# Kernel tuning notes

Hardware: AMD Instinct MI355X
Metric: run time of the kernel (lower is better)

The kernel has to match this reference:

```python
import jax, jax.numpy as jnp
import numpy as np

N_NODES = 100000
N_HEDGES = 200000
N_INC = 1000000
N_GRAPHS = 256
H = 64        # h_dim
HE = 35       # hedge_fea_dim
HOUT = 128    # hout_dim
NL = 3        # n_layers
EPS = 1e-5


def _segment_mean(vals, idx, num_segments):
    s = jax.ops.segment_sum(vals, idx, num_segments=num_segments)
    cnt = jax.ops.segment_sum(jnp.ones((vals.shape[0],), vals.dtype), idx,
                              num_segments=num_segments)
    return s / jnp.maximum(cnt, 1.0)[:, None]


def _bn(z, g, b):
    # training-mode BatchNorm1d: batch stats, biased variance
    m = jnp.mean(z, axis=0)
    v = jnp.var(z, axis=0)
    return (z - m) * jax.lax.rsqrt(v + EPS) * g + b


def setup_inputs() -> dict:
    key = jax.random.key(0)
    ks = jax.random.split(key, 32)
    inp = {
        "x": jax.random.normal(ks[0], (N_NODES, 92), jnp.float32),
        "node_idx": jax.random.randint(ks[1], (N_INC,), 0, N_NODES),
        "hedge_idx": jax.random.randint(ks[2], (N_INC,), 0, N_HEDGES),
        "hedge_attr": jax.random.normal(ks[3], (N_HEDGES, HE), jnp.float32),
        "batch": jnp.sort(jax.random.randint(ks[4], (N_NODES,), 0, N_GRAPHS)),
    }
    s = 0.05
    cat = H + HE  # 99
    inp["embed_w"] = jax.random.normal(ks[5], (92, H), jnp.float32) * s
    inp["embed_b"] = jnp.zeros((H,), jnp.float32)
    inp["f1_w"] = jax.random.normal(ks[6], (NL, cat, HE), jnp.float32) * s
    inp["f1_b"] = jnp.zeros((NL, HE), jnp.float32)
    inp["c1_w"] = jax.random.normal(ks[7], (NL, cat, HE), jnp.float32) * s
    inp["c1_b"] = jnp.zeros((NL, HE), jnp.float32)
    inp["f2_w"] = jax.random.normal(ks[8], (NL, cat, H), jnp.float32) * s
    inp["f2_b"] = jnp.zeros((NL, H), jnp.float32)
    inp["c2_w"] = jax.random.normal(ks[9], (NL, cat, H), jnp.float32) * s
    inp["c2_b"] = jnp.zeros((NL, H), jnp.float32)
    inp["bnf_g"] = jnp.ones((NL, HE), jnp.float32)
    inp["bnf_b"] = jnp.zeros((NL, HE), jnp.float32)
    inp["bnc_g"] = jnp.ones((NL, HE), jnp.float32)
    inp["bnc_b"] = jnp.zeros((NL, HE), jnp.float32)
    inp["bno_g"] = jnp.ones((NL, H), jnp.float32)
    inp["bno_b"] = jnp.zeros((NL, H), jnp.float32)
    inp["l2_w"] = jax.random.normal(ks[10], (H, HOUT), jnp.float32) * s
    inp["l2_b"] = jnp.zeros((HOUT,), jnp.float32)
    inp["out_w"] = jax.random.normal(ks[11], (HOUT, 1), jnp.float32) * s
    inp["out_b"] = jnp.zeros((1,), jnp.float32)
    return inp


def reference(x, node_idx, hedge_idx, hedge_attr, batch,
              embed_w, embed_b, f1_w, f1_b, c1_w, c1_b,
              f2_w, f2_b, c2_w, c2_b,
              bnf_g, bnf_b, bnc_g, bnc_b, bno_g, bno_b,
              l2_w, l2_b, out_w, out_b):
    sp = jax.nn.softplus
    x = x @ embed_w + embed_b  # [N, H]
    for i in range(NL):
        # gather node feats per incidence, mean over each hyperedge
        hx = _segment_mean(x[node_idx], hedge_idx, N_HEDGES)       # [NH, H]
        msg = jnp.concatenate([hx, hedge_attr], axis=1)            # [NH, H+HE]
        z_f = _bn(msg @ f1_w[i] + f1_b[i], bnf_g[i], bnf_b[i])
        z_c = _bn(msg @ c1_w[i] + c1_b[i], bnc_g[i], bnc_b[i])
        hedge_attr = jax.nn.sigmoid(z_f) * sp(z_c)                 # [NH, HE]
        z = jnp.concatenate([x[node_idx], hedge_attr[hedge_idx]], axis=-1)  # [E, H+HE]
        o = jax.nn.sigmoid(z @ f2_w[i] + f2_b[i]) * sp(z @ c2_w[i] + c2_b[i])  # [E, H]
        o = _segment_mean(o, node_idx, N_NODES)                    # [N, H]
        o = _bn(o, bno_g[i], bno_b[i])
        x = sp(o + x)
    pooled = _segment_mean(x, batch, N_GRAPHS)                     # [G, H]
    h = sp(pooled @ l2_w + l2_b)                                   # [G, HOUT]
    return h @ out_w + out_b                                       # [G, 1]
```

## Files before the change

### kernel.cpp

```cpp
#include <hip/hip_runtime.h>
#include <math.h>

#define N_NODES 100000
#define N_HEDGES 200000
#define N_INC 1000000
#define N_GRAPHS 256
#define HD 64
#define HE 35
#define CAT 99
#define EPSB 1e-5f

typedef __attribute__((ext_vector_type(8))) short short8;
typedef __attribute__((ext_vector_type(4))) float f32x4;

__device__ __forceinline__ float sp_f(float x) {
  return fmaxf(x, 0.f) + __logf(1.f + __expf(-fabsf(x)));
}
__device__ __forceinline__ float sig_f(float x) {
  return __builtin_amdgcn_rcpf(1.f + __expf(-x));
}
__device__ __forceinline__ unsigned bfr(float x) {
  unsigned u = __float_as_uint(x);
  return (u + 0x7fffu + ((u >> 16) & 1u)) >> 16;
}
__device__ __forceinline__ unsigned pk2(float lo, float hi) {
  return bfr(lo) | (bfr(hi) << 16);
}
__device__ __forceinline__ float blo(unsigned v) { return __uint_as_float(v << 16); }
__device__ __forceinline__ float bhi(unsigned v) {
  return __uint_as_float(v & 0xffff0000u);
}
__device__ __forceinline__ float bf2f(unsigned short s) {
  return __uint_as_float(((unsigned)s) << 16);
}

__global__ __launch_bounds__(256) void k_hist(const int* __restrict__ nidx,
                                              const int* __restrict__ hidx,
                                              int* __restrict__ degN,
                                              int* __restrict__ degH) {
  int e = blockIdx.x * 256 + threadIdx.x;
  if (e >= N_INC) return;
  atomicAdd(&degH[hidx[e]], 1);
  atomicAdd(&degN[nidx[e]], 1);
}

__global__ __launch_bounds__(256) void k_alloc(const int* __restrict__ deg, int n,
                                               int* __restrict__ off,
                                               int* __restrict__ cur,
                                               int* __restrict__ gctr) {
  __shared__ int s[256];
  __shared__ int base;
  int t = threadIdx.x;
  int i = blockIdx.x * 256 + t;
  int d = (i < n) ? deg[i] : 0;
  s[t] = d;
  __syncthreads();
  for (int st = 1; st < 256; st <<= 1) {
    int u = 0;
    if (t >= st) u = s[t - st];
    __syncthreads();
    if (t >= st) s[t] += u;
    __syncthreads();
  }
  if (t == 255) base = atomicAdd(gctr, s[255]);
  __syncthreads();
  int ex = s[t] - d + base;
  if (i < n) {
    off[i] = ex;
    cur[i] = ex;
  }
}

__global__ __launch_bounds__(256) void k_fill(const int* __restrict__ nidx,
                                              const int* __restrict__ hidx,
                                              int* __restrict__ curH,
                                              int* __restrict__ curN,
                                              int* __restrict__ permHn,
                                              int* __restrict__ permNh) {
  int e = blockIdx.x * 256 + threadIdx.x;
  if (e >= N_INC) return;
  int nd = nidx[e], hg = hidx[e];
  int p = atomicAdd(&curH[hg], 1);
  permHn[p] = nd;
  int q = atomicAdd(&curN[nd], 1);
  permNh[q] = hg;
}

__global__ __launch_bounds__(64) void k_wpack(const float* __restrict__ f1w,
                                              const float* __restrict__ c1w,
                                              uint4* __restrict__ wpk) {
  int b = blockIdx.x;
  int layer = b / 20, rem = b % 20, ct = rem / 4, ks = rem % 4;
  int lane = threadIdx.x;
  int col = ct * 16 + (lane & 15);
  int k0 = ks * 32 + (lane >> 4) * 8;
  const float* wf = f1w + layer * CAT * HE;
  const float* wc = c1w + layer * CAT * HE;
  unsigned v[4];
#pragma unroll
  for (int p = 0; p < 4; ++p) {
    float lo = 0.f, hi = 0.f;
    int ka = k0 + p * 2, kb = ka + 1;
    if (ka < 99) {
      if (col < 35) lo = wf[ka * 35 + col];
      else if (col >= 36 && col < 71) lo = wc[ka * 35 + (col - 36)];
    }
    if (kb < 99) {
      if (col < 35) hi = wf[kb * 35 + col];
      else if (col >= 36 && col < 71) hi = wc[kb * 35 + (col - 36)];
    }
    v[p] = pk2(lo, hi);
  }
  uint4 o;
  o.x = v[0]; o.y = v[1]; o.z = v[2]; o.w = v[3];
  wpk[b * 64 + lane] = o;
}

__global__ __launch_bounds__(256) void k_cvt_ha(const float* __restrict__ src,
                                                unsigned short* __restrict__ dst,
                                                int n) {
  int t = blockIdx.x * 256 + threadIdx.x;
  if (t < n) dst[t] = (unsigned short)bfr(src[t]);
}

__global__ __launch_bounds__(256) void k_embed(const float* __restrict__ x,
                                               const float* __restrict__ w,
                                               const float* __restrict__ b,
                                               float* __restrict__ out,
                                               unsigned short* __restrict__ outb) {
  __shared__ float ws[92 * 64];
  __shared__ float rs[16][93];
  int tid = threadIdx.x;
  for (int i = tid; i < 92 * 64; i += 256) ws[i] = w[i];
  int r0 = blockIdx.x * 16;
  for (int i = tid; i < 16 * 92; i += 256) {
    int r = i / 92, k = i - r * 92;
    rs[r][k] = x[(r0 + r) * 92 + k];
  }
  __syncthreads();
  int h = tid & 63;
  float bias = b[h];
  for (int rr = tid >> 6; rr < 16; rr += 4) {
    float acc = bias;
    for (int k = 0; k < 92; ++k) acc += rs[rr][k] * ws[k * 64 + h];
    out[(r0 + rr) * 64 + h] = acc;
    outb[(r0 + rr) * 64 + h] = (unsigned short)bfr(acc);
  }
}

__global__ __launch_bounds__(256) void k_gather_hx(
    const unsigned short* __restrict__ xb, const int* __restrict__ permHn,
    const int* __restrict__ offH, const int* __restrict__ degH,
    unsigned short* __restrict__ hxb) {
  int gt = blockIdx.x * 256 + threadIdx.x;
  int wid = gt >> 6, h = gt & 63;
  if (wid >= N_HEDGES) return;
  int o = offH[wid], d = degH[wid];
  float acc = 0.f;
  int k = 0;
  for (; k + 4 <= d; k += 4) {
    int n0 = permHn[o + k], n1 = permHn[o + k + 1];
    int n2 = permHn[o + k + 2], n3 = permHn[o + k + 3];
    float a0 = bf2f(xb[n0 * 64 + h]);
    float a1 = bf2f(xb[n1 * 64 + h]);
    float a2 = bf2f(xb[n2 * 64 + h]);
    float a3 = bf2f(xb[n3 * 64 + h]);
    acc += (a0 + a1) + (a2 + a3);
  }
  for (; k < d; ++k) acc += bf2f(xb[permHn[o + k] * 64 + h]);
  hxb[wid * 64 + h] = (unsigned short)bfr(acc / (float)max(d, 1));
}

#define GR 128
__global__ __launch_bounds__(256) void k_hedge_gemm(
    const unsigned short* __restrict__ hxb, const unsigned short* __restrict__ hab,
    const uint4* __restrict__ wpk, float* __restrict__ z,
    float* __restrict__ stats) {
  __shared__ unsigned short msg[GR * 128];
  __shared__ float ps[160];
  int tid = threadIdx.x;
  int w = tid >> 6, lane = tid & 63;
  int r0 = blockIdx.x * GR;
  if (tid < 160) ps[tid] = 0.f;

  short8 bfg[5][4];
#pragma unroll
  for (int ct = 0; ct < 5; ++ct)
#pragma unroll
    for (int ks = 0; ks < 4; ++ks)
      bfg[ct][ks] = __builtin_bit_cast(short8, wpk[(ct * 4 + ks) * 64 + lane]);

  char* mb = (char*)msg;
  for (int i = tid; i < GR * 16; i += 256) {
    int r = i >> 4, c4 = (i & 15) * 4;
    int row = r0 + r;
    ushort4 v;
    if (row < N_HEDGES)
      v = *(const ushort4*)(hxb + (size_t)row * 64 + c4);
    else
      v.x = v.y = v.z = v.w = 0;
    int byte = r * 256 + c4 * 2;
    *(ushort4*)(mb + (byte ^ ((r & 7) << 4))) = v;
  }
  for (int i = tid; i < GR * 64; i += 256) {
    int r = i >> 6, c = 64 + (i & 63);
    int row = r0 + r;
    unsigned short v = 0;
    if (row < N_HEDGES && c < 99) v = hab[(size_t)row * 35 + (c - 64)];
    int byte = r * 256 + c * 2;
    *(unsigned short*)(mb + (byte ^ ((r & 7) << 4))) = v;
  }
  __syncthreads();

#pragma unroll
  for (int rt = 0; rt < 2; ++rt) {
    int rloc = w * 32 + rt * 16 + (lane & 15);
    short8 a[4];
#pragma unroll
    for (int ks = 0; ks < 4; ++ks) {
      int byte = rloc * 256 + (ks * 32 + (lane >> 4) * 8) * 2;
      a[ks] = *(const short8*)(mb + (byte ^ ((rloc & 7) << 4)));
    }
#pragma unroll
    for (int ct = 0; ct < 5; ++ct) {
      f32x4 acc = {0.f, 0.f, 0.f, 0.f};
#pragma unroll
      for (int ks = 0; ks < 4; ++ks)
        acc = __builtin_amdgcn_mfma_f32_16x16x32_bf16(a[ks], bfg[ct][ks], acc, 0, 0, 0);
      float s = (acc[0] + acc[1]) + (acc[2] + acc[3]);
      float q = (acc[0] * acc[0] + acc[1] * acc[1]) +
                (acc[2] * acc[2] + acc[3] * acc[3]);
      s += __shfl_xor(s, 16);
      s += __shfl_xor(s, 32);
      q += __shfl_xor(q, 16);
      q += __shfl_xor(q, 32);
      int col = ct * 16 + (lane & 15);
      if ((lane >> 4) == 0 && col < 72) {
        atomicAdd(&ps[col], s);
        atomicAdd(&ps[80 + col], q);
      }
      int growb = r0 + w * 32 + rt * 16 + ((lane >> 4) << 2);
      if (col < 72) {
#pragma unroll
        for (int r = 0; r < 4; ++r) {
          int grow = growb + r;
          if (grow < N_HEDGES) z[(size_t)grow * 72 + col] = acc[r];
        }
      }
    }
  }
  __syncthreads();
  if (tid < 160) atomicAdd(&stats[tid], ps[tid]);
}

__global__ __launch_bounds__(256) void k_hedge_apply(
    const float* __restrict__ z, const float* __restrict__ stats,
    const float* __restrict__ gf, const float* __restrict__ bf_,
    const float* __restrict__ gc, const float* __restrict__ bc_,
    unsigned short* __restrict__ hab) {
  int t = blockIdx.x * 256 + threadIdx.x;
  if (t >= N_HEDGES * 35) return;
  int r = t / 35, c = t - r * 35;
  const float inv = 1.f / N_HEDGES;
  float mf = stats[c] * inv;
  float vf = stats[80 + c] * inv - mf * mf;
  float mc = stats[36 + c] * inv;
  float vc = stats[116 + c] * inv - mc * mc;
  const float* zr = &z[(size_t)r * 72];
  float nf = (zr[c] - mf) * rsqrtf(vf + EPSB) * gf[c] + bf_[c];
  float nc = (zr[36 + c] - mc) * rsqrtf(vc + EPSB) * gc[c] + bc_[c];
  hab[t] = (unsigned short)bfr(sig_f(nf) * sp_f(nc));
}

__global__ __launch_bounds__(256) void k_uv_node(const float* __restrict__ x,
                                                 const float* __restrict__ f2w,
                                                 const float* __restrict__ c2w,
                                                 unsigned* __restrict__ Ufc) {
  __shared__ float wf[64 * 64];
  __shared__ float wc[64 * 64];
  __shared__ float rs[16][65];
  int tid = threadIdx.x;
  for (int i = tid; i < 64 * 64; i += 256) {
    wf[i] = f2w[i];
    wc[i] = c2w[i];
  }
  int r0 = blockIdx.x * 16;
  for (int i = tid; i < 16 * 64; i += 256) {
    int r = i >> 6, k = i & 63;
    rs[r][k] = x[(r0 + r) * 64 + k];
  }
  __syncthreads();
  int h = tid & 63, rb = tid >> 6;
  float af0 = 0, af1 = 0, af2 = 0, af3 = 0, ac0 = 0, ac1 = 0, ac2 = 0, ac3 = 0;
  for (int k = 0; k < 64; ++k) {
    float wfv = wf[k * 64 + h], wcv = wc[k * 64 + h];
    float m0 = rs[rb][k], m1 = rs[rb + 4][k], m2 = rs[rb + 8][k], m3 = rs[rb + 12][k];
    af0 += m0 * wfv; ac0 += m0 * wcv;
    af1 += m1 * wfv; ac1 += m1 * wcv;
    af2 += m2 * wfv; ac2 += m2 * wcv;
    af3 += m3 * wfv; ac3 += m3 * wcv;
  }
  int row = r0 + rb;
  Ufc[row * 64 + h] = pk2(af0, ac0);
  Ufc[(row + 4) * 64 + h] = pk2(af1, ac1);
  Ufc[(row + 8) * 64 + h] = pk2(af2, ac2);
  Ufc[(row + 12) * 64 + h] = pk2(af3, ac3);
}

__global__ __launch_bounds__(256) void k_uv_hedge(
    const unsigned short* __restrict__ hab, const float* __restrict__ f2wb,
    const float* __restrict__ c2wb, const float* __restrict__ f2b,
    const float* __restrict__ c2b, unsigned* __restrict__ Vfc) {
  __shared__ float wf[35 * 64];
  __shared__ float wc[35 * 64];
  __shared__ float rs[16][36];
  int tid = threadIdx.x;
  for (int i = tid; i < 35 * 64; i += 256) {
    wf[i] = f2wb[i];
    wc[i] = c2wb[i];
  }
  int r0 = blockIdx.x * 16;
  for (int i = tid; i < 16 * 35; i += 256) {
    int r = i / 35, k = i - r * 35;
    rs[r][k] = bf2f(hab[(r0 + r) * 35 + k]);
  }
  __syncthreads();
  int h = tid & 63, rb = tid >> 6;
  float af0, af1, af2, af3, ac0, ac1, ac2, ac3;
  af0 = af1 = af2 = af3 = f2b[h];
  ac0 = ac1 = ac2 = ac3 = c2b[h];
  for (int k = 0; k < 35; ++k) {
    float wfv = wf[k * 64 + h], wcv = wc[k * 64 + h];
    float m0 = rs[rb][k], m1 = rs[rb + 4][k], m2 = rs[rb + 8][k], m3 = rs[rb + 12][k];
    af0 += m0 * wfv; ac0 += m0 * wcv;
    af1 += m1 * wfv; ac1 += m1 * wcv;
    af2 += m2 * wfv; ac2 += m2 * wcv;
    af3 += m3 * wfv; ac3 += m3 * wcv;
  }
  int row = r0 + rb;
  Vfc[row * 64 + h] = pk2(af0, ac0);
  Vfc[(row + 4) * 64 + h] = pk2(af1, ac1);
  Vfc[(row + 8) * 64 + h] = pk2(af2, ac2);
  Vfc[(row + 12) * 64 + h] = pk2(af3, ac3);
}

__device__ __forceinline__ float act2(float uf, float uc, unsigned v) {
  float a = uf + blo(v);
  float b = uc + bhi(v);
  return sig_f(a) * sp_f(b);
}
__global__ __launch_bounds__(256) void k_node_aggr(const int* __restrict__ permNh,
                                                   const int* __restrict__ offN,
                                                   const int* __restrict__ degN,
                                                   const unsigned* __restrict__ Ufc,
                                                   const unsigned* __restrict__ Vfc,
                                                   float* __restrict__ o) {
  int gt = blockIdx.x * 256 + threadIdx.x;
  int wid = gt >> 6, h = gt & 63;
  if (wid >= N_NODES) return;
  int off = offN[wid], d = degN[wid];
  unsigned u = Ufc[wid * 64 + h];
  float uf = blo(u), uc = bhi(u);
  float acc = 0.f;
  int k = 0;
  for (; k + 4 <= d; k += 4) {
    int h0 = permNh[off + k], h1 = permNh[off + k + 1];
    int h2 = permNh[off + k + 2], h3 = permNh[off + k + 3];
    unsigned v0 = Vfc[h0 * 64 + h];
    unsigned v1 = Vfc[h1 * 64 + h];
    unsigned v2 = Vfc[h2 * 64 + h];
    unsigned v3 = Vfc[h3 * 64 + h];
    acc += (act2(uf, uc, v0) + act2(uf, uc, v1)) +
           (act2(uf, uc, v2) + act2(uf, uc, v3));
  }
  for (; k < d; ++k) acc += act2(uf, uc, Vfc[permNh[off + k] * 64 + h]);
  o[wid * 64 + h] = acc / (float)max(d, 1);
}

__global__ __launch_bounds__(256) void k_ostats(const float* __restrict__ o,
                                                float* __restrict__ stats) {
  int h = threadIdx.x & 63;
  int rs = threadIdx.x >> 6;
  float s = 0.f, sq = 0.f;
  for (int r = blockIdx.x * 4 + rs; r < N_NODES; r += gridDim.x * 4) {
    float v = o[r * 64 + h];
    s += v;
    sq += v * v;
  }
  __shared__ float ls[4][2][64];
  ls[rs][0][h] = s;
  ls[rs][1][h] = sq;
  __syncthreads();
  if (threadIdx.x < 64) {
    float ts = ls[0][0][h] + ls[1][0][h] + ls[2][0][h] + ls[3][0][h];
    float tq = ls[0][1][h] + ls[1][1][h] + ls[2][1][h] + ls[3][1][h];
    atomicAdd(&stats[h], ts);
    atomicAdd(&stats[64 + h], tq);
  }
}

__global__ __launch_bounds__(256) void k_update(float* __restrict__ x,
                                                unsigned short* __restrict__ xb,
                                                const float* __restrict__ o,
                                                const float* __restrict__ stats,
                                                const float* __restrict__ g,
                                                const float* __restrict__ b) {
  int t = blockIdx.x * 256 + threadIdx.x;
  int h = t & 63;
  float mean = stats[h] * (1.f / N_NODES);
  float var = stats[64 + h] * (1.f / N_NODES) - mean * mean;
  float is = rsqrtf(var + EPSB);
  float v = (o[t] - mean) * is * g[h] + b[h];
  float r = sp_f(v + x[t]);
  x[t] = r;
  xb[t] = (unsigned short)bfr(r);
}

#define PR 512
__global__ __launch_bounds__(256) void k_pool(const float* __restrict__ x,
                                              const int* __restrict__ batch,
                                              float* __restrict__ pooled,
                                              float* __restrict__ gcnt) {
  int h = threadIdx.x & 63, rs = threadIdx.x >> 6;
  int r0 = blockIdx.x * PR;
  int rend = min(r0 + PR, N_NODES);
  int gcur = -1;
  float acc = 0.f;
  int cnt = 0;
  for (int r = r0 + rs; r < rend; r += 4) {
    int g = batch[r];
    if (g != gcur) {
      if (gcur >= 0) {
        atomicAdd(&pooled[gcur * 64 + h], acc);
        if (h == 0) atomicAdd(&gcnt[gcur], (float)cnt);
      }
      gcur = g;
      acc = 0.f;
      cnt = 0;
    }
    acc += x[r * 64 + h];
    cnt++;
  }
  if (gcur >= 0) {
    atomicAdd(&pooled[gcur * 64 + h], acc);
    if (h == 0) atomicAdd(&gcnt[gcur], (float)cnt);
  }
}

__global__ __launch_bounds__(128) void k_final(const float* __restrict__ pooled,
                                               const float* __restrict__ gcnt,
                                               const float* __restrict__ l2w,
                                               const float* __restrict__ l2b,
                                               const float* __restrict__ ow,
                                               const float* __restrict__ ob,
                                               float* __restrict__ out) {
  int g = blockIdx.x;
  int t = threadIdx.x;
  __shared__ float row[64];
  __shared__ float hh[128];
  if (t < 64) row[t] = pooled[g * 64 + t] / fmaxf(gcnt[g], 1.f);
  __syncthreads();
  float acc = l2b[t];
  for (int k = 0; k < 64; ++k) acc += row[k] * l2w[k * 128 + t];
  hh[t] = sp_f(acc) * ow[t];
  __syncthreads();
  for (int s = 64; s > 0; s >>= 1) {
    if (t < s) hh[t] += hh[t + s];
    __syncthreads();
  }
  if (t == 0) out[g] = hh[0] + ob[0];
}

extern "C" void kernel_launch(void* const* d_in, const int* in_sizes, int n_in,
                              void* d_out, int out_size, void* d_ws, size_t ws_size,
                              hipStream_t stream) {
  const float* x_in = (const float*)d_in[0];
  const int* node_idx = (const int*)d_in[1];
  const int* hedge_idx = (const int*)d_in[2];
  const float* hedge_attr = (const float*)d_in[3];
  const int* batch = (const int*)d_in[4];
  const float* embed_w = (const float*)d_in[5];
  const float* embed_b = (const float*)d_in[6];
  const float* f1_w = (const float*)d_in[7];
  const float* c1_w = (const float*)d_in[9];
  const float* f2_w = (const float*)d_in[11];
  const float* f2_b = (const float*)d_in[12];
  const float* c2_w = (const float*)d_in[13];
  const float* c2_b = (const float*)d_in[14];
  const float* bnf_g = (const float*)d_in[15];
  const float* bnf_b = (const float*)d_in[16];
  const float* bnc_g = (const float*)d_in[17];
  const float* bnc_b = (const float*)d_in[18];
  const float* bno_g = (const float*)d_in[19];
  const float* bno_b = (const float*)d_in[20];
  const float* l2_w = (const float*)d_in[21];
  const float* l2_b = (const float*)d_in[22];
  const float* out_w = (const float*)d_in[23];
  const float* out_b = (const float*)d_in[24];

  char* base = (char*)d_ws;
  size_t off = 0;
  auto alloc = [&](size_t bytes) {
    size_t o = off;
    off = (off + bytes + 255) & ~(size_t)255;
    return o;
  };
  float* xbuf = (float*)(base + alloc((size_t)N_NODES * 64 * 4));
  unsigned short* xbf = (unsigned short*)(base + alloc((size_t)N_NODES * 64 * 2));
  unsigned short* hxb = (unsigned short*)(base + alloc((size_t)N_HEDGES * 64 * 2));
  unsigned short* hab = (unsigned short*)(base + alloc((size_t)N_HEDGES * 35 * 2));
  unsigned* Vfc = (unsigned*)(base + alloc((size_t)N_HEDGES * 64 * 4));
  float* obuf = (float*)(base + alloc((size_t)N_NODES * 64 * 4));
  float* zbuf = (float*)Vfc;
  unsigned* Ufc = (unsigned*)(base + alloc((size_t)N_NODES * 64 * 4));
  uint4* wpk = (uint4*)(base + alloc((size_t)60 * 64 * 16));
  float* hstats = (float*)(base + alloc(160 * 4));
  float* ostats = (float*)(base + alloc(128 * 4));
  float* pooled = (float*)(base + alloc((size_t)N_GRAPHS * 64 * 4));
  float* gcnt = (float*)(base + alloc((size_t)N_GRAPHS * 4));
  int* degH = (int*)(base + alloc((size_t)N_HEDGES * 4));
  int* offH = (int*)(base + alloc((size_t)N_HEDGES * 4));
  int* curH = (int*)(base + alloc((size_t)N_HEDGES * 4));
  int* degN = (int*)(base + alloc((size_t)N_NODES * 4));
  int* offN = (int*)(base + alloc((size_t)N_NODES * 4));
  int* curN = (int*)(base + alloc((size_t)N_NODES * 4));
  int* permHn = (int*)(base + alloc((size_t)N_INC * 4));
  int* permNh = (int*)(base + alloc((size_t)N_INC * 4));
  int* gctr = (int*)(base + alloc(2 * 4));
  (void)ws_size;
  (void)in_sizes;
  (void)n_in;
  (void)out_size;

  hipMemsetAsync(degH, 0, (size_t)N_HEDGES * 4, stream);
  hipMemsetAsync(degN, 0, (size_t)N_NODES * 4, stream);
  hipMemsetAsync(gctr, 0, 2 * 4, stream);
  k_hist<<<(N_INC + 255) / 256, 256, 0, stream>>>(node_idx, hedge_idx, degN, degH);
  k_alloc<<<(N_HEDGES + 255) / 256, 256, 0, stream>>>(degH, N_HEDGES, offH, curH, &gctr[0]);
  k_alloc<<<(N_NODES + 255) / 256, 256, 0, stream>>>(degN, N_NODES, offN, curN, &gctr[1]);
  k_fill<<<(N_INC + 255) / 256, 256, 0, stream>>>(node_idx, hedge_idx, curH, curN,
                                                  permHn, permNh);
  k_wpack<<<60, 64, 0, stream>>>(f1_w, c1_w, wpk);
  k_cvt_ha<<<(N_HEDGES * 35 + 255) / 256, 256, 0, stream>>>(hedge_attr, hab,
                                                            N_HEDGES * 35);

  k_embed<<<N_NODES / 16, 256, 0, stream>>>(x_in, embed_w, embed_b, xbuf, xbf);

  for (int i = 0; i < 3; ++i) {
    k_gather_hx<<<N_HEDGES * 64 / 256, 256, 0, stream>>>(xbf, permHn, offH, degH, hxb);

    hipMemsetAsync(hstats, 0, 160 * 4, stream);
    k_hedge_gemm<<<(N_HEDGES + GR - 1) / GR, 256, 0, stream>>>(
        hxb, hab, wpk + (size_t)i * 20 * 64, zbuf, hstats);
    k_hedge_apply<<<(N_HEDGES * 35 + 255) / 256, 256, 0, stream>>>(
        zbuf, hstats, bnf_g + i * HE, bnf_b + i * HE, bnc_g + i * HE, bnc_b + i * HE,
        hab);

    k_uv_node<<<N_NODES / 16, 256, 0, stream>>>(xbuf, f2_w + i * CAT * 64,
                                                c2_w + i * CAT * 64, Ufc);
    k_uv_hedge<<<N_HEDGES / 16, 256, 0, stream>>>(
        hab, f2_w + i * CAT * 64 + 64 * 64, c2_w + i * CAT * 64 + 64 * 64,
        f2_b + i * 64, c2_b + i * 64, Vfc);

    k_node_aggr<<<N_NODES * 64 / 256, 256, 0, stream>>>(permNh, offN, degN, Ufc, Vfc,
                                                        obuf);

    hipMemsetAsync(ostats, 0, 128 * 4, stream);
    k_ostats<<<1024, 256, 0, stream>>>(obuf, ostats);
    k_update<<<N_NODES * 64 / 256, 256, 0, stream>>>(xbuf, xbf, obuf, ostats,
                                                     bno_g + i * 64, bno_b + i * 64);
  }

  hipMemsetAsync(pooled, 0, (size_t)N_GRAPHS * 64 * 4, stream);
  hipMemsetAsync(gcnt, 0, (size_t)N_GRAPHS * 4, stream);
  k_pool<<<(N_NODES + PR - 1) / PR, 256, 0, stream>>>(xbuf, batch, pooled, gcnt);
  k_final<<<N_GRAPHS, 128, 0, stream>>>(pooled, gcnt, l2_w, l2_b, out_w, out_b,
                                        (float*)d_out);
}
```

Measured before the change: 1.460 ms.

## Fuse hyperedge gather into GEMM, drop fp32 node state, batch memsets and CSR build

The hyperedge mean-gather is moved into the hedge GEMM kernel, which now writes the averaged node features straight into shared memory, so the hx intermediate buffer and its separate launch are gone. The fp32 copy of the node state is removed and every consumer reads the bf16 buffer. That cuts memory traffic but makes the residual accumulate in bf16, which lowers precision. The CSR build records each incidence's rank during the histogram, so the fill step no longer needs atomics, and the two prefix-scan launches become one. The many small memsets are merged into a few contiguous ones, and the per-layer stats move into preallocated slices.

After: 1.386 ms. -5.1%, faster.

```diff
diff --git a/kernel.cpp b/kernel.cpp
--- a/kernel.cpp
+++ b/kernel.cpp
@@ -37,21 +37,34 @@
 __global__ __launch_bounds__(256) void k_hist(const int* __restrict__ nidx,
                                               const int* __restrict__ hidx,
                                               int* __restrict__ degN,
-                                              int* __restrict__ degH) {
+                                              int* __restrict__ degH,
+                                              int* __restrict__ rankN,
+                                              int* __restrict__ rankH) {
   int e = blockIdx.x * 256 + threadIdx.x;
   if (e >= N_INC) return;
-  atomicAdd(&degH[hidx[e]], 1);
-  atomicAdd(&degN[nidx[e]], 1);
-}
-
-__global__ __launch_bounds__(256) void k_alloc(const int* __restrict__ deg, int n,
-                                               int* __restrict__ off,
-                                               int* __restrict__ cur,
-                                               int* __restrict__ gctr) {
+  rankH[e] = atomicAdd(&degH[hidx[e]], 1);
+  rankN[e] = atomicAdd(&degN[nidx[e]], 1);
+}
+
+#define CHB ((N_HEDGES + 255) / 256)
+#define CNB ((N_NODES + 255) / 256)
+__global__ __launch_bounds__(256) void k_alloc2(const int* __restrict__ degH,
+                                                const int* __restrict__ degN,
+                                                int* __restrict__ offH,
+                                                int* __restrict__ offN,
+                                                int* __restrict__ gctr) {
   __shared__ int s[256];
   __shared__ int base;
-  int t = threadIdx.x;
-  int i = blockIdx.x * 256 + t;
+  int b = blockIdx.x, t = threadIdx.x;
+  const int* deg;
+  int* off;
+  int n, i;
+  int* ctr;
+  if (b < CHB) {
+    deg = degH; off = offH; n = N_HEDGES; ctr = &gctr[0]; i = b * 256 + t;
+  } else {
+    deg = degN; off = offN; n = N_NODES; ctr = &gctr[1]; i = (b - CHB) * 256 + t;
+  }
   int d = (i < n) ? deg[i] : 0;
   s[t] = d;
   __syncthreads();
@@ -62,28 +75,24 @@
     if (t >= st) s[t] += u;
     __syncthreads();
   }
-  if (t == 255) base = atomicAdd(gctr, s[255]);
-  __syncthreads();
-  int ex = s[t] - d + base;
-  if (i < n) {
-    off[i] = ex;
-    cur[i] = ex;
-  }
+  if (t == 255) base = atomicAdd(ctr, s[255]);
+  __syncthreads();
+  if (i < n) off[i] = s[t] - d + base;
 }
 
 __global__ __launch_bounds__(256) void k_fill(const int* __restrict__ nidx,
                                               const int* __restrict__ hidx,
-                                              int* __restrict__ curH,
-                                              int* __restrict__ curN,
+                                              const int* __restrict__ rankH,
+                                              const int* __restrict__ rankN,
+                                              const int* __restrict__ offH,
+                                              const int* __restrict__ offN,
                                               int* __restrict__ permHn,
                                               int* __restrict__ permNh) {
   int e = blockIdx.x * 256 + threadIdx.x;
   if (e >= N_INC) return;
   int nd = nidx[e], hg = hidx[e];
-  int p = atomicAdd(&curH[hg], 1);
-  permHn[p] = nd;
-  int q = atomicAdd(&curN[nd], 1);
-  permNh[q] = hg;
+  permHn[offH[hg] + rankH[e]] = nd;
+  permNh[offN[nd] + rankN[e]] = hg;
 }
 
 __global__ __launch_bounds__(64) void k_wpack(const float* __restrict__ f1w,
@@ -126,7 +135,6 @@
 __global__ __launch_bounds__(256) void k_embed(const float* __restrict__ x,
                                                const float* __restrict__ w,
                                                const float* __restrict__ b,
-                                               float* __restrict__ out,
                                                unsigned short* __restrict__ outb) {
   __shared__ float ws[92 * 64];
   __shared__ float rs[16][93];
@@ -143,39 +151,16 @@
   for (int rr = tid >> 6; rr < 16; rr += 4) {
     float acc = bias;
     for (int k = 0; k < 92; ++k) acc += rs[rr][k] * ws[k * 64 + h];
-    out[(r0 + rr) * 64 + h] = acc;
     outb[(r0 + rr) * 64 + h] = (unsigned short)bfr(acc);
   }
 }
 
-__global__ __launch_bounds__(256) void k_gather_hx(
+#define GR 128
+__global__ __launch_bounds__(256) void k_hedge_gemm(
     const unsigned short* __restrict__ xb, const int* __restrict__ permHn,
     const int* __restrict__ offH, const int* __restrict__ degH,
-    unsigned short* __restrict__ hxb) {
-  int gt = blockIdx.x * 256 + threadIdx.x;
-  int wid = gt >> 6, h = gt & 63;
-  if (wid >= N_HEDGES) return;
-  int o = offH[wid], d = degH[wid];
-  float acc = 0.f;
-  int k = 0;
-  for (; k + 4 <= d; k += 4) {
-    int n0 = permHn[o + k], n1 = permHn[o + k + 1];
-    int n2 = permHn[o + k + 2], n3 = permHn[o + k + 3];
-    float a0 = bf2f(xb[n0 * 64 + h]);
-    float a1 = bf2f(xb[n1 * 64 + h]);
-    float a2 = bf2f(xb[n2 * 64 + h]);
-    float a3 = bf2f(xb[n3 * 64 + h]);
-    acc += (a0 + a1) + (a2 + a3);
-  }
-  for (; k < d; ++k) acc += bf2f(xb[permHn[o + k] * 64 + h]);
-  hxb[wid * 64 + h] = (unsigned short)bfr(acc / (float)max(d, 1));
-}
-
-#define GR 128
-__global__ __launch_bounds__(256) void k_hedge_gemm(
-    const unsigned short* __restrict__ hxb, const unsigned short* __restrict__ hab,
-    const uint4* __restrict__ wpk, float* __restrict__ z,
-    float* __restrict__ stats) {
+    const unsigned short* __restrict__ hab, const uint4* __restrict__ wpk,
+    float* __restrict__ z, float* __restrict__ stats) {
   __shared__ unsigned short msg[GR * 128];
   __shared__ float ps[160];
   int tid = threadIdx.x;
@@ -191,24 +176,27 @@
       bfg[ct][ks] = __builtin_bit_cast(short8, wpk[(ct * 4 + ks) * 64 + lane]);
 
   char* mb = (char*)msg;
-  for (int i = tid; i < GR * 16; i += 256) {
-    int r = i >> 4, c4 = (i & 15) * 4;
-    int row = r0 + r;
-    ushort4 v;
-    if (row < N_HEDGES)
-      v = *(const ushort4*)(hxb + (size_t)row * 64 + c4);
-    else
-      v.x = v.y = v.z = v.w = 0;
-    int byte = r * 256 + c4 * 2;
-    *(ushort4*)(mb + (byte ^ ((r & 7) << 4))) = v;
-  }
-  for (int i = tid; i < GR * 64; i += 256) {
-    int r = i >> 6, c = 64 + (i & 63);
-    int row = r0 + r;
-    unsigned short v = 0;
-    if (row < N_HEDGES && c < 99) v = hab[(size_t)row * 35 + (c - 64)];
-    int byte = r * 256 + c * 2;
-    *(unsigned short*)(mb + (byte ^ ((r & 7) << 4))) = v;
+  for (int r = 0; r < 32; ++r) {
+    int rloc = w * 32 + r;
+    int row = r0 + rloc;
+    float acc = 0.f;
+    unsigned short hv = 0;
+    if (row < N_HEDGES) {
+      int o = offH[row], d = degH[row];
+      int k = 0;
+      for (; k + 4 <= d; k += 4) {
+        int n0 = permHn[o + k], n1 = permHn[o + k + 1];
+        int n2 = permHn[o + k + 2], n3 = permHn[o + k + 3];
+        acc += (bf2f(xb[(size_t)n0 * 64 + lane]) + bf2f(xb[(size_t)n1 * 64 + lane])) +
+               (bf2f(xb[(size_t)n2 * 64 + lane]) + bf2f(xb[(size_t)n3 * 64 + lane]));
+      }
+      for (; k < d; ++k) acc += bf2f(xb[(size_t)permHn[o + k] * 64 + lane]);
+      acc *= 1.f / (float)max(d, 1);
+      if (lane < 35) hv = hab[(size_t)row * 35 + lane];
+    }
+    int swz = (rloc & 7) << 4;
+    *(unsigned short*)(mb + ((rloc * 256 + lane * 2) ^ swz)) = (unsigned short)bfr(acc);
+    *(unsigned short*)(mb + ((rloc * 256 + 128 + lane * 2) ^ swz)) = hv;
   }
   __syncthreads();
 
@@ -272,7 +260,7 @@
   hab[t] = (unsigned short)bfr(sig_f(nf) * sp_f(nc));
 }
 
-__global__ __launch_bounds__(256) void k_uv_node(const float* __restrict__ x,
+__global__ __launch_bounds__(256) void k_uv_node(const unsigned short* __restrict__ xb,
                                                  const float* __restrict__ f2w,
                                                  const float* __restrict__ c2w,
                                                  unsigned* __restrict__ Ufc) {
@@ -287,7 +275,7 @@
   int r0 = blockIdx.x * 16;
   for (int i = tid; i < 16 * 64; i += 256) {
     int r = i >> 6, k = i & 63;
-    rs[r][k] = x[(r0 + r) * 64 + k];
+    rs[r][k] = bf2f(xb[(size_t)(r0 + r) * 64 + k]);
   }
   __syncthreads();
   int h = tid & 63, rb = tid >> 6;
@@ -399,8 +387,7 @@
   }
 }
 
-__global__ __launch_bounds__(256) void k_update(float* __restrict__ x,
-                                                unsigned short* __restrict__ xb,
+__global__ __launch_bounds__(256) void k_update(unsigned short* __restrict__ xb,
                                                 const float* __restrict__ o,
                                                 const float* __restrict__ stats,
                                                 const float* __restrict__ g,
@@ -411,13 +398,12 @@
   float var = stats[64 + h] * (1.f / N_NODES) - mean * mean;
   float is = rsqrtf(var + EPSB);
   float v = (o[t] - mean) * is * g[h] + b[h];
-  float r = sp_f(v + x[t]);
-  x[t] = r;
+  float r = sp_f(v + bf2f(xb[t]));
   xb[t] = (unsigned short)bfr(r);
 }
 
 #define PR 512
-__global__ __launch_bounds__(256) void k_pool(const float* __restrict__ x,
+__global__ __launch_bounds__(256) void k_pool(const unsigned short* __restrict__ xb,
                                               const int* __restrict__ batch,
                                               float* __restrict__ pooled,
                                               float* __restrict__ gcnt) {
@@ -438,7 +424,7 @@
       acc = 0.f;
       cnt = 0;
     }
-    acc += x[r * 64 + h];
+    acc += bf2f(xb[(size_t)r * 64 + h]);
     cnt++;
   }
   if (gcur >= 0) {
@@ -505,58 +491,56 @@
     off = (off + bytes + 255) & ~(size_t)255;
     return o;
   };
-  float* xbuf = (float*)(base + alloc((size_t)N_NODES * 64 * 4));
   unsigned short* xbf = (unsigned short*)(base + alloc((size_t)N_NODES * 64 * 2));
-  unsigned short* hxb = (unsigned short*)(base + alloc((size_t)N_HEDGES * 64 * 2));
   unsigned short* hab = (unsigned short*)(base + alloc((size_t)N_HEDGES * 35 * 2));
   unsigned* Vfc = (unsigned*)(base + alloc((size_t)N_HEDGES * 64 * 4));
   float* obuf = (float*)(base + alloc((size_t)N_NODES * 64 * 4));
   float* zbuf = (float*)Vfc;
   unsigned* Ufc = (unsigned*)(base + alloc((size_t)N_NODES * 64 * 4));
   uint4* wpk = (uint4*)(base + alloc((size_t)60 * 64 * 16));
-  float* hstats = (float*)(base + alloc(160 * 4));
-  float* ostats = (float*)(base + alloc(128 * 4));
+  float* hstatsA = (float*)(base + alloc(3 * 160 * 4));
+  float* ostatsA = (float*)(base + alloc(3 * 128 * 4));
   float* pooled = (float*)(base + alloc((size_t)N_GRAPHS * 64 * 4));
   float* gcnt = (float*)(base + alloc((size_t)N_GRAPHS * 4));
   int* degH = (int*)(base + alloc((size_t)N_HEDGES * 4));
+  int* degN = (int*)(base + alloc((size_t)N_NODES * 4));
+  int* gctr = (int*)(base + alloc(2 * 4));
   int* offH = (int*)(base + alloc((size_t)N_HEDGES * 4));
-  int* curH = (int*)(base + alloc((size_t)N_HEDGES * 4));
-  int* degN = (int*)(base + alloc((size_t)N_NODES * 4));
   int* offN = (int*)(base + alloc((size_t)N_NODES * 4));
-  int* curN = (int*)(base + alloc((size_t)N_NODES * 4));
+  int* rankH = (int*)(base + alloc((size_t)N_INC * 4));
+  int* rankN = (int*)(base + alloc((size_t)N_INC * 4));
   int* permHn = (int*)(base + alloc((size_t)N_INC * 4));
   int* permNh = (int*)(base + alloc((size_t)N_INC * 4));
-  int* gctr = (int*)(base + alloc(2 * 4));
   (void)ws_size;
   (void)in_sizes;
   (void)n_in;
   (void)out_size;
 
-  hipMemsetAsync(degH, 0, (size_t)N_HEDGES * 4, stream);
-  hipMemsetAsync(degN, 0, (size_t)N_NODES * 4, stream);
-  hipMemsetAsync(gctr, 0, 2 * 4, stream);
-  k_hist<<<(N_INC + 255) / 256, 256, 0, stream>>>(node_idx, hedge_idx, degN, degH);
-  k_alloc<<<(N_HEDGES + 255) / 256, 256, 0, stream>>>(degH, N_HEDGES, offH, curH, &gctr[0]);
-  k_alloc<<<(N_NODES + 255) / 256, 256, 0, stream>>>(degN, N_NODES, offN, curN, &gctr[1]);
-  k_fill<<<(N_INC + 255) / 256, 256, 0, stream>>>(node_idx, hedge_idx, curH, curN,
-                                                  permHn, permNh);
+  hipMemsetAsync(degH, 0, (size_t)((char*)gctr - (char*)degH) + 2 * 4, stream);
+  k_hist<<<(N_INC + 255) / 256, 256, 0, stream>>>(node_idx, hedge_idx, degN, degH,
+                                                  rankN, rankH);
+  k_alloc2<<<CHB + CNB, 256, 0, stream>>>(degH, degN, offH, offN, gctr);
+  k_fill<<<(N_INC + 255) / 256, 256, 0, stream>>>(node_idx, hedge_idx, rankH, rankN,
+                                                  offH, offN, permHn, permNh);
   k_wpack<<<60, 64, 0, stream>>>(f1_w, c1_w, wpk);
   k_cvt_ha<<<(N_HEDGES * 35 + 255) / 256, 256, 0, stream>>>(hedge_attr, hab,
                                                             N_HEDGES * 35);
-
-  k_embed<<<N_NODES / 16, 256, 0, stream>>>(x_in, embed_w, embed_b, xbuf, xbf);
+  k_embed<<<N_NODES / 16, 256, 0, stream>>>(x_in, embed_w, embed_b, xbf);
+
+  hipMemsetAsync(hstatsA, 0, (size_t)((char*)ostatsA - (char*)hstatsA) + 3 * 128 * 4,
+                 stream);
 
   for (int i = 0; i < 3; ++i) {
-    k_gather_hx<<<N_HEDGES * 64 / 256, 256, 0, stream>>>(xbf, permHn, offH, degH, hxb);
-
-    hipMemsetAsync(hstats, 0, 160 * 4, stream);
+    float* hstats = hstatsA + i * 160;
+    float* ostats = ostatsA + i * 128;
+
     k_hedge_gemm<<<(N_HEDGES + GR - 1) / GR, 256, 0, stream>>>(
-        hxb, hab, wpk + (size_t)i * 20 * 64, zbuf, hstats);
+        xbf, permHn, offH, degH, hab, wpk + (size_t)i * 20 * 64, zbuf, hstats);
     k_hedge_apply<<<(N_HEDGES * 35 + 255) / 256, 256, 0, stream>>>(
         zbuf, hstats, bnf_g + i * HE, bnf_b + i * HE, bnc_g + i * HE, bnc_b + i * HE,
         hab);
 
-    k_uv_node<<<N_NODES / 16, 256, 0, stream>>>(xbuf, f2_w + i * CAT * 64,
+    k_uv_node<<<N_NODES / 16, 256, 0, stream>>>(xbf, f2_w + i * CAT * 64,
                                                 c2_w + i * CAT * 64, Ufc);
     k_uv_hedge<<<N_HEDGES / 16, 256, 0, stream>>>(
         hab, f2_w + i * CAT * 64 + 64 * 64, c2_w + i * CAT * 64 + 64 * 64,
@@ -565,15 +549,14 @@
     k_node_aggr<<<N_NODES * 64 / 256, 256, 0, stream>>>(permNh, offN, degN, Ufc, Vfc,
                                                         obuf);
 
-    hipMemsetAsync(ostats, 0, 128 * 4, stream);
     k_ostats<<<1024, 256, 0, stream>>>(obuf, ostats);
-    k_update<<<N_NODES * 64 / 256, 256, 0, stream>>>(xbuf, xbf, obuf, ostats,
+    k_update<<<N_NODES * 64 / 256, 256, 0, stream>>>(xbf, obuf, ostats,
                                                      bno_g + i * 64, bno_b + i * 64);
   }
 
-  hipMemsetAsync(pooled, 0, (size_t)N_GRAPHS * 64 * 4, stream);
-  hipMemsetAsync(gcnt, 0, (size_t)N_GRAPHS * 4, stream);
-  k_pool<<<(N_NODES + PR - 1) / PR, 256, 0, stream>>>(xbuf, batch, pooled, gcnt);
+  hipMemsetAsync(pooled, 0, (size_t)((char*)gcnt - (char*)pooled) + N_GRAPHS * 4,
+                 stream);
+  k_pool<<<(N_NODES + PR - 1) / PR, 256, 0, stream>>>(xbf, batch, pooled, gcnt);
   k_final<<<N_GRAPHS, 128, 0, stream>>>(pooled, gcnt, l2_w, l2_b, out_w, out_b,
                                         (float*)d_out);
 }
```
